# Kernel optimization log

Hardware: AMD Instinct MI355X
Metric: run time of the kernel (lower is better)

The kernel has to match this reference:

```python
import jax, jax.numpy as jnp
import numpy as np

B, T, M, P, Y_DIM = 1024, 128, 256, 256, 1


def setup_inputs() -> dict:
    key = jax.random.key(0)
    ks = jax.random.split(key, 12)
    s = 0.05
    return {
        "Y": jax.random.normal(ks[0], (B, T - 1, Y_DIM), jnp.float32),
        "X_encoded": jax.random.normal(ks[1], (T, B, M), jnp.float32),
        # attention params (torch Linear weight layout: (out, in), no bias)
        "WU_d": jax.random.normal(ks[2], (M, 2 * P + M), jnp.float32) * s,
        "v_d": jax.random.normal(ks[3], (1, M), jnp.float32) * s,
        "Wl": jax.random.normal(ks[4], (1, Y_DIM + M), jnp.float32) * s,
        # LSTM(1, p) params, pytorch gate order i,f,g,o
        "W_ih": jax.random.normal(ks[5], (4 * P, 1), jnp.float32) * s,
        "W_hh": jax.random.normal(ks[6], (4 * P, P), jnp.float32) * s,
        "b_ih": jax.random.normal(ks[7], (4 * P,), jnp.float32) * s,
        "b_hh": jax.random.normal(ks[8], (4 * P,), jnp.float32) * s,
        # output head (with bias)
        "Wb_w": jax.random.normal(ks[9], (P, P + M), jnp.float32) * s,
        "Wb_b": jnp.zeros((P,), jnp.float32),
        "vb_w": jax.random.normal(ks[10], (Y_DIM, P), jnp.float32) * s,
        "vb_b": jnp.zeros((Y_DIM,), jnp.float32),
    }


def _decode(Y, X_encoded, WU_d, v_d, Wl, W_ih, W_hh, b_ih, b_hh, Wb_w, Wb_b, vb_w, vb_b):
    X_bt = jnp.transpose(X_encoded, (1, 0, 2))  # (B, T, m)
    b = Y.shape[0]

    def step(carry, y_t):
        h, c, _ = carry  # h,c: (B, p)
        d = jnp.concatenate([h, c], axis=-1)  # (B, 2p)
        d_rep = jnp.broadcast_to(d[:, None, :], (b, T, 2 * P))
        z = jnp.concatenate([d_rep, X_bt], axis=-1)  # (B, T, 2p+m)
        l = jnp.einsum('btm,om->bto', jnp.tanh(jnp.einsum('btk,mk->btm', z, WU_d)), v_d)[..., 0]  # (B, T)
        beta = jax.nn.softmax(l, axis=1)
        ctx = jnp.einsum('bt,btm->bm', beta, X_bt)  # (B, m)
        y_tilde = jnp.concatenate([y_t, ctx], axis=-1) @ Wl.T  # (B, 1)
        gates = y_tilde @ W_ih.T + h @ W_hh.T + b_ih + b_hh  # (B, 4p)
        i_g, f_g, g_g, o_g = jnp.split(gates, 4, axis=-1)
        c_new = jax.nn.sigmoid(f_g) * c + jax.nn.sigmoid(i_g) * jnp.tanh(g_g)
        h_new = jax.nn.sigmoid(o_g) * jnp.tanh(c_new)
        return (h_new, c_new, ctx), None

    init = (jnp.zeros((b, P), Y.dtype), jnp.zeros((b, P), Y.dtype), jnp.zeros((b, M), Y.dtype))
    (h, c, ctx), _ = jax.lax.scan(step, init, jnp.transpose(Y, (1, 0, 2)))  # scan over T-1 steps
    hc = jnp.concatenate([h, ctx], axis=-1)  # (B, p+m)
    return (hc @ Wb_w.T + Wb_b) @ vb_w.T + vb_b  # (B, y_dim)


def reference(Y, X_encoded, WU_d, v_d, Wl, W_ih, W_hh, b_ih, b_hh, Wb_w, Wb_b, vb_w, vb_b):
    return _decode(Y, X_encoded, WU_d, v_d, Wl, W_ih, W_hh, b_ih, b_hh, Wb_w, Wb_b, vb_w, vb_b)
```

## Files before the change

### kernel.cpp

```cpp
#include <hip/hip_runtime.h>


#define B_SZ 1024
#define T_SZ 128
#define M_SZ 256
#define NSTEP 127

typedef __attribute__((ext_vector_type(8))) short short8;
typedef __attribute__((ext_vector_type(4))) float f32x4;

__device__ __forceinline__ float bf2f_lo(unsigned u) {
  return __builtin_bit_cast(float, u << 16);
}
__device__ __forceinline__ float bf2f_hi(unsigned u) {
  return __builtin_bit_cast(float, u & 0xffff0000u);
}
__device__ __forceinline__ unsigned short f2bf(float f) {
  unsigned u = __builtin_bit_cast(unsigned, f);
  u = (u + 0x7fffu + ((u >> 16) & 1u)) >> 16;
  return (unsigned short)u;
}
__device__ __forceinline__ float fexp2(float x) { return __builtin_amdgcn_exp2f(x); }
__device__ __forceinline__ float frcp(float x) { return __builtin_amdgcn_rcpf(x); }
__device__ __forceinline__ float tanh_f(float x) {
  float t = fexp2(x * 2.8853900817779268f);
  return 1.f - 2.f * frcp(t + 1.f);
}
__device__ __forceinline__ float sigm_f(float x) {
  return frcp(1.f + fexp2(x * -1.4426950408889634f));
}
__device__ __forceinline__ short8 as_s8(uint4 u) { return __builtin_bit_cast(short8, u); }

__global__ void prep_w(const float* __restrict__ WU_d,
                       const float* __restrict__ W_hh,
                       const float* __restrict__ b_ih,
                       const float* __restrict__ b_hh,
                       unsigned short* __restrict__ W1F,
                       unsigned short* __restrict__ W2F,
                       unsigned short* __restrict__ WxF,
                       float* __restrict__ bsum) {
  int i = blockIdx.x * 256 + threadIdx.x;
  if (i < 131072) {
    int j = i & 7, lane = (i >> 3) & 63, ks = (i >> 9) & 15, mt = i >> 13;
    int r = lane & 15, kg = lane >> 4;
    int k = ks * 32 + kg * 8 + j;
    W1F[i] = f2bf(WU_d[(mt * 16 + r) * 768 + k]);
  } else if (i < 131072 + 262144) {
    int i2 = i - 131072;
    int j = i2 & 7, lane = (i2 >> 3) & 63, ks = (i2 >> 9) & 7, jt = i2 >> 12;
    int r = lane & 15, kg = lane >> 4;
    int k = ks * 32 + kg * 8 + j;
    W2F[i2] = f2bf(W_hh[(jt * 16 + r) * 256 + k]);
  } else if (i < 131072 + 262144 + 65536) {
    int i3 = i - (131072 + 262144);
    int j = i3 & 7, lane = (i3 >> 3) & 63, ks = (i3 >> 9) & 7, mt = i3 >> 12;
    int r = lane & 15, kg = lane >> 4;
    int k = 512 + ks * 32 + kg * 8 + j;
    WxF[i3] = f2bf(WU_d[(mt * 16 + r) * 768 + k]);
  } else if (i < 131072 + 262144 + 65536 + 1024) {
    int i4 = i - (131072 + 262144 + 65536);
    bsum[i4] = b_ih[i4] + b_hh[i4];
  }
}

__global__ __launch_bounds__(256, 1) void prep_xw(
    const float* __restrict__ X,
    const unsigned short* __restrict__ WxF,
    const float* __restrict__ Wl,
    unsigned short* __restrict__ XW,
    float* __restrict__ XWl) {
  __shared__ __align__(16) unsigned short XL[128 * 256];
  const int b = blockIdx.x, tid = threadIdx.x;
  for (int i = tid; i < 128 * 256; i += 256) {
    int t = i >> 8, k = i & 255;
    XL[i] = f2bf(X[(size_t)t * 262144 + (size_t)b * 256 + k]);
  }
  __syncthreads();
  const int wave = tid >> 6, lane = tid & 63, r = lane & 15, kg = lane >> 4;
  for (int tt = 0; tt < 8; ++tt) {
    uint4 a[8];
#pragma unroll
    for (int ks = 0; ks < 8; ++ks)
      a[ks] = *(const uint4*)&XL[(tt * 16 + r) * 256 + ks * 32 + kg * 8];
#pragma unroll
    for (int mtl = 0; mtl < 4; ++mtl) {
      const int mt = wave * 4 + mtl;
      f32x4 acc = {0.f, 0.f, 0.f, 0.f};
#pragma unroll
      for (int ks = 0; ks < 8; ++ks) {
        uint4 braw = *(const uint4*)(WxF + ((size_t)(mt * 8 + ks) * 64 + lane) * 8);
        acc = __builtin_amdgcn_mfma_f32_16x16x32_bf16(as_s8(a[ks]), as_s8(braw), acc, 0, 0, 0);
      }
#pragma unroll
      for (int rr = 0; rr < 4; ++rr) {
        int trow = tt * 16 + kg * 4 + rr;
        XW[(size_t)b * 32768 + trow * 256 + mt * 16 + r] = f2bf(acc[rr]);
      }
    }
  }
  float wl4[4];
#pragma unroll
  for (int j = 0; j < 4; ++j) wl4[j] = Wl[1 + lane * 4 + j];
  for (int t = wave * 32; t < wave * 32 + 32; ++t) {
    uint2 q = *(const uint2*)&XL[t * 256 + lane * 4];
    float s = wl4[0] * bf2f_lo(q.x) + wl4[1] * bf2f_hi(q.x) +
              wl4[2] * bf2f_lo(q.y) + wl4[3] * bf2f_hi(q.y);
#pragma unroll
    for (int off = 1; off < 64; off <<= 1) s += __shfl_xor(s, off, 64);
    if (lane == 0) XWl[b * 128 + t] = s;
  }
}

__global__ __launch_bounds__(1024, 4) void scan_k(
    const float* __restrict__ Yg,
    const float* __restrict__ X,
    const unsigned short* __restrict__ XW,
    const float* __restrict__ XWl,
    const unsigned short* __restrict__ W1F,
    const unsigned short* __restrict__ W2F,
    const float* __restrict__ bsum,
    const float* __restrict__ v_d,
    const float* __restrict__ Wl,
    const float* __restrict__ W_ih,
    const float* __restrict__ Wb_w,
    const float* __restrict__ Wb_b,
    const float* __restrict__ vb_w,
    const float* __restrict__ vb_b,
    float* __restrict__ outp) {
  __shared__ __align__(16) unsigned short hcbf[16][520];
  __shared__ __align__(16) float dWL[4][256];
  __shared__ float gL[4][1024];
  __shared__ float lL[4][128];
  __shared__ float betaL[4][128];
  __shared__ float ctxW[4][4][256];
  __shared__ float ctxL[4][256];
  __shared__ float ytL[4];

  const int tid = threadIdx.x;
  const int wave = tid >> 6;
  const int lane = tid & 63;
  const int r = lane & 15;
  const int kg = lane >> 4;
  const int b0 = blockIdx.x * 4;
  const int bb = wave >> 2;
  const int tw = wave & 3;
  const int lp = tid & 255;
  const int lb = tid >> 8;
  const int m8 = (lane & 31) * 8;
  const int th = lane >> 5;

  for (int i = tid; i < 16 * 520; i += 1024) (&hcbf[0][0])[i] = 0;

  float v8[8];
#pragma unroll
  for (int j = 0; j < 8; ++j) v8[j] = v_d[m8 + j];
  float wih4g[4], bs4g[4];
#pragma unroll
  for (int g = 0; g < 4; ++g) { wih4g[g] = W_ih[g * 256 + lp]; bs4g[g] = bsum[g * 256 + lp]; }
  const float wl0 = Wl[0];
  float c_reg = 0.f;

  const unsigned short* XWb = XW + (size_t)(b0 + bb) * (T_SZ * M_SZ);
  const float* Yb = Yg + (size_t)(b0 + wave) * NSTEP;
  const float* XWlb = XWl + (size_t)(b0 + wave) * T_SZ;

  __syncthreads();

  for (int step = 0; step < NSTEP; ++step) {
    {
      const int mt = wave;
      f32x4 acc = {0.f, 0.f, 0.f, 0.f};
      const unsigned short* bp = W1F + ((size_t)(mt * 16) * 64 + lane) * 8;
#pragma unroll
      for (int ks = 0; ks < 16; ++ks) {
        uint4 a = *(const uint4*)&hcbf[r][ks * 32 + kg * 8];
        uint4 braw = *(const uint4*)(bp + (size_t)ks * 512);
        acc = __builtin_amdgcn_mfma_f32_16x16x32_bf16(as_s8(a), as_s8(braw), acc, 0, 0, 0);
      }
      if (kg == 0) {
#pragma unroll
        for (int rr = 0; rr < 4; ++rr) dWL[rr][mt * 16 + r] = acc[rr];
      }
    }
    __syncthreads();

    {
      float dw8[8];
      *(f32x4*)&dw8[0] = *(const f32x4*)&dWL[bb][m8];
      *(f32x4*)&dw8[4] = *(const f32x4*)&dWL[bb][m8 + 4];
      const unsigned short* p = XWb + (tw * 32 + th) * M_SZ + m8;
#pragma unroll 8
      for (int i = 0; i < 16; ++i) {
        uint4 q = *(const uint4*)(p + i * 512);
        float s = v8[0] * tanh_f(dw8[0] + bf2f_lo(q.x)) + v8[1] * tanh_f(dw8[1] + bf2f_hi(q.x)) +
                  v8[2] * tanh_f(dw8[2] + bf2f_lo(q.y)) + v8[3] * tanh_f(dw8[3] + bf2f_hi(q.y)) +
                  v8[4] * tanh_f(dw8[4] + bf2f_lo(q.z)) + v8[5] * tanh_f(dw8[5] + bf2f_hi(q.z)) +
                  v8[6] * tanh_f(dw8[6] + bf2f_lo(q.w)) + v8[7] * tanh_f(dw8[7] + bf2f_hi(q.w));
#pragma unroll
        for (int off = 1; off < 32; off <<= 1) s += __shfl_xor(s, off, 64);
        if ((lane & 31) == 0) lL[bb][tw * 32 + 2 * i + th] = s;
      }
    }
    __syncthreads();

    if (wave < 4) {
      float l0 = lL[wave][lane], l1 = lL[wave][64 + lane];
      float mx = fmaxf(l0, l1);
#pragma unroll
      for (int off = 1; off < 64; off <<= 1) mx = fmaxf(mx, __shfl_xor(mx, off, 64));
      float e0 = fexp2((l0 - mx) * 1.4426950408889634f);
      float e1 = fexp2((l1 - mx) * 1.4426950408889634f);
      float sm = e0 + e1;
      float yt = e0 * XWlb[lane] + e1 * XWlb[64 + lane];
#pragma unroll
      for (int off = 1; off < 64; off <<= 1) {
        sm += __shfl_xor(sm, off, 64);
        yt += __shfl_xor(yt, off, 64);
      }
      float inv = frcp(sm);
      betaL[wave][lane] = e0 * inv;
      betaL[wave][64 + lane] = e1 * inv;
      if (lane == 0) ytL[wave] = yt * inv + wl0 * Yb[step];
    }

    {
#pragma unroll
      for (int jtl = 0; jtl < 4; ++jtl) {
        const int jt = wave * 4 + jtl;
        f32x4 acc = {0.f, 0.f, 0.f, 0.f};
        const unsigned short* bp = W2F + ((size_t)(jt * 8) * 64 + lane) * 8;
#pragma unroll
        for (int ks = 0; ks < 8; ++ks) {
          uint4 a = *(const uint4*)&hcbf[r][ks * 32 + kg * 8];
          uint4 braw = *(const uint4*)(bp + (size_t)ks * 512);
          acc = __builtin_amdgcn_mfma_f32_16x16x32_bf16(as_s8(a), as_s8(braw), acc, 0, 0, 0);
        }
        if (kg == 0) {
#pragma unroll
          for (int rr = 0; rr < 4; ++rr) gL[rr][jt * 16 + r] = acc[rr];
        }
      }
    }
    __syncthreads();

    if (step == NSTEP - 1) {
      const int m4 = lane * 4;
      f32x4 c4 = {0.f, 0.f, 0.f, 0.f};
      for (int t = tw * 32; t < tw * 32 + 32; ++t) {
        float bta = betaL[bb][t];
        f32x4 x4 = *(const f32x4*)&X[(size_t)t * 262144 + (size_t)(b0 + bb) * 256 + m4];
        c4.x += bta * x4.x;
        c4.y += bta * x4.y;
        c4.z += bta * x4.z;
        c4.w += bta * x4.w;
      }
      *(f32x4*)&ctxW[bb][tw][m4] = c4;
    }

    {
      float yt = ytL[lb];
      float ig = gL[lb][lp] + yt * wih4g[0] + bs4g[0];
      float fg = gL[lb][256 + lp] + yt * wih4g[1] + bs4g[1];
      float gg = gL[lb][512 + lp] + yt * wih4g[2] + bs4g[2];
      float og = gL[lb][768 + lp] + yt * wih4g[3] + bs4g[3];
      float cn = sigm_f(fg) * c_reg + sigm_f(ig) * tanh_f(gg);
      float hn = sigm_f(og) * tanh_f(cn);
      c_reg = cn;
      hcbf[lb][lp] = f2bf(hn);
      hcbf[lb][256 + lp] = f2bf(cn);
    }
    __syncthreads();
  }

  ctxL[lb][lp] = ctxW[lb][0][lp] + ctxW[lb][1][lp] + ctxW[lb][2][lp] + ctxW[lb][3][lp];
  __syncthreads();

  if (wave < 4) {
    const int m4 = lane * 4;
    float h0 = 0.f, h1 = 0.f, h2 = 0.f, h3 = 0.f;
    for (int q = 0; q < 512; ++q) {
      float hcq = (q < 256) ? bf2f_lo((unsigned)hcbf[wave][q]) : ctxL[wave][q - 256];
      const float* wb = Wb_w + (size_t)m4 * 512 + q;
      h0 += hcq * wb[0];
      h1 += hcq * wb[512];
      h2 += hcq * wb[1024];
      h3 += hcq * wb[1536];
    }
    float o = (h0 + Wb_b[m4]) * vb_w[m4] + (h1 + Wb_b[m4 + 1]) * vb_w[m4 + 1] +
              (h2 + Wb_b[m4 + 2]) * vb_w[m4 + 2] + (h3 + Wb_b[m4 + 3]) * vb_w[m4 + 3];
#pragma unroll
    for (int off = 1; off < 64; off <<= 1) o += __shfl_xor(o, off, 64);
    if (lane == 0) outp[b0 + wave] = o + vb_b[0];
  }
}

extern "C" void kernel_launch(void* const* d_in, const int* in_sizes, int n_in,
                              void* d_out, int out_size, void* d_ws, size_t ws_size,
                              hipStream_t stream) {
  const float* Y = (const float*)d_in[0];
  const float* X = (const float*)d_in[1];
  const float* WU_d = (const float*)d_in[2];
  const float* v_d = (const float*)d_in[3];
  const float* Wl = (const float*)d_in[4];
  const float* W_ih = (const float*)d_in[5];
  const float* W_hh = (const float*)d_in[6];
  const float* b_ih = (const float*)d_in[7];
  const float* b_hh = (const float*)d_in[8];
  const float* Wb_w = (const float*)d_in[9];
  const float* Wb_b = (const float*)d_in[10];
  const float* vb_w = (const float*)d_in[11];
  const float* vb_b = (const float*)d_in[12];

  char* ws = (char*)d_ws;
  unsigned short* XW = (unsigned short*)(ws + 0);
  float* XWl = (float*)(ws + 67108864);
  unsigned short* W1F = (unsigned short*)(ws + 67633152);
  unsigned short* W2F = (unsigned short*)(ws + 67895296);
  unsigned short* WxF = (unsigned short*)(ws + 68419584);
  float* bsum = (float*)(ws + 68550656);

  prep_w<<<1796, 256, 0, stream>>>(WU_d, W_hh, b_ih, b_hh, W1F, W2F, WxF, bsum);
  prep_xw<<<1024, 256, 0, stream>>>(X, WxF, Wl, XW, XWl);
  scan_k<<<256, 1024, 0, stream>>>(Y, X, XW, XWl, W1F, W2F, bsum, v_d, Wl, W_ih,
                                   Wb_w, Wb_b, vb_w, vb_b, (float*)d_out);
}
```

Measured before the change: 6.008 ms.

## Process two batch rows per block to launch 512 scan blocks

Each 1024-thread scan block now handles 2 batch rows instead of 4, doubling the grid to 512 blocks so all CUs on the device get work. Eight waves now split the 128 time positions per row. Y and XWl per-row values are preloaded into shared memory, and XW and X streaming reads use nontemporal loads. The trade-off is that the per-step MFMA work on W1F/W2F is repeated for fewer rows, so the weight traffic per row roughly doubles and half the MFMA tile rows are wasted.

```diff
diff --git a/kernel.cpp b/kernel.cpp
--- a/kernel.cpp
+++ b/kernel.cpp
@@ -8,6 +8,7 @@
 
 typedef __attribute__((ext_vector_type(8))) short short8;
 typedef __attribute__((ext_vector_type(4))) float f32x4;
+typedef __attribute__((ext_vector_type(4))) unsigned int u32x4;
 
 __device__ __forceinline__ float bf2f_lo(unsigned u) {
   return __builtin_bit_cast(float, u << 16);
@@ -111,7 +112,7 @@
   }
 }
 
-__global__ __launch_bounds__(1024, 4) void scan_k(
+__global__ __launch_bounds__(1024, 8) void scan_k(
     const float* __restrict__ Yg,
     const float* __restrict__ X,
     const unsigned short* __restrict__ XW,
@@ -128,28 +129,38 @@
     const float* __restrict__ vb_b,
     float* __restrict__ outp) {
   __shared__ __align__(16) unsigned short hcbf[16][520];
-  __shared__ __align__(16) float dWL[4][256];
-  __shared__ float gL[4][1024];
-  __shared__ float lL[4][128];
-  __shared__ float betaL[4][128];
-  __shared__ float ctxW[4][4][256];
-  __shared__ float ctxL[4][256];
-  __shared__ float ytL[4];
+  __shared__ __align__(16) float dWL[2][256];
+  __shared__ float gL[2][1024];
+  __shared__ float lL[2][128];
+  __shared__ float betaL[2][128];
+  __shared__ float ctxW[2][8][256];
+  __shared__ float ctxL[2][256];
+  __shared__ float YL[2][128];
+  __shared__ float XWlL[2][128];
+  __shared__ float ytL[2];
 
   const int tid = threadIdx.x;
   const int wave = tid >> 6;
   const int lane = tid & 63;
   const int r = lane & 15;
   const int kg = lane >> 4;
-  const int b0 = blockIdx.x * 4;
-  const int bb = wave >> 2;
-  const int tw = wave & 3;
+  const int b0 = blockIdx.x * 2;
+  const int bb = wave >> 3;
+  const int tw = wave & 7;
   const int lp = tid & 255;
   const int lb = tid >> 8;
   const int m8 = (lane & 31) * 8;
   const int th = lane >> 5;
 
   for (int i = tid; i < 16 * 520; i += 1024) (&hcbf[0][0])[i] = 0;
+  if (tid < 254) {
+    int b2 = tid / 127, st = tid % 127;
+    YL[b2][st] = Yg[(size_t)(b0 + b2) * NSTEP + st];
+  }
+  if (tid >= 512 && tid < 768) {
+    int i2 = tid - 512, b2 = i2 >> 7, t = i2 & 127;
+    XWlL[b2][t] = XWl[(size_t)(b0 + b2) * T_SZ + t];
+  }
 
   float v8[8];
 #pragma unroll
@@ -161,8 +172,6 @@
   float c_reg = 0.f;
 
   const unsigned short* XWb = XW + (size_t)(b0 + bb) * (T_SZ * M_SZ);
-  const float* Yb = Yg + (size_t)(b0 + wave) * NSTEP;
-  const float* XWlb = XWl + (size_t)(b0 + wave) * T_SZ;
 
   __syncthreads();
 
@@ -178,8 +187,8 @@
         acc = __builtin_amdgcn_mfma_f32_16x16x32_bf16(as_s8(a), as_s8(braw), acc, 0, 0, 0);
       }
       if (kg == 0) {
-#pragma unroll
-        for (int rr = 0; rr < 4; ++rr) dWL[rr][mt * 16 + r] = acc[rr];
+        dWL[0][mt * 16 + r] = acc[0];
+        dWL[1][mt * 16 + r] = acc[1];
       }
     }
     __syncthreads();
@@ -188,22 +197,22 @@
       float dw8[8];
       *(f32x4*)&dw8[0] = *(const f32x4*)&dWL[bb][m8];
       *(f32x4*)&dw8[4] = *(const f32x4*)&dWL[bb][m8 + 4];
-      const unsigned short* p = XWb + (tw * 32 + th) * M_SZ + m8;
-#pragma unroll 8
-      for (int i = 0; i < 16; ++i) {
-        uint4 q = *(const uint4*)(p + i * 512);
+      const unsigned short* p = XWb + (tw * 16 + th) * M_SZ + m8;
+#pragma unroll
+      for (int i = 0; i < 8; ++i) {
+        u32x4 q = __builtin_nontemporal_load((const u32x4*)(p + i * 512));
         float s = v8[0] * tanh_f(dw8[0] + bf2f_lo(q.x)) + v8[1] * tanh_f(dw8[1] + bf2f_hi(q.x)) +
                   v8[2] * tanh_f(dw8[2] + bf2f_lo(q.y)) + v8[3] * tanh_f(dw8[3] + bf2f_hi(q.y)) +
                   v8[4] * tanh_f(dw8[4] + bf2f_lo(q.z)) + v8[5] * tanh_f(dw8[5] + bf2f_hi(q.z)) +
                   v8[6] * tanh_f(dw8[6] + bf2f_lo(q.w)) + v8[7] * tanh_f(dw8[7] + bf2f_hi(q.w));
 #pragma unroll
         for (int off = 1; off < 32; off <<= 1) s += __shfl_xor(s, off, 64);
-        if ((lane & 31) == 0) lL[bb][tw * 32 + 2 * i + th] = s;
+        if ((lane & 31) == 0) lL[bb][tw * 16 + 2 * i + th] = s;
       }
     }
     __syncthreads();
 
-    if (wave < 4) {
+    if (wave < 2) {
       float l0 = lL[wave][lane], l1 = lL[wave][64 + lane];
       float mx = fmaxf(l0, l1);
 #pragma unroll
@@ -211,7 +220,7 @@
       float e0 = fexp2((l0 - mx) * 1.4426950408889634f);
       float e1 = fexp2((l1 - mx) * 1.4426950408889634f);
       float sm = e0 + e1;
-      float yt = e0 * XWlb[lane] + e1 * XWlb[64 + lane];
+      float yt = e0 * XWlL[wave][lane] + e1 * XWlL[wave][64 + lane];
 #pragma unroll
       for (int off = 1; off < 64; off <<= 1) {
         sm += __shfl_xor(sm, off, 64);
@@ -220,7 +229,7 @@
       float inv = frcp(sm);
       betaL[wave][lane] = e0 * inv;
       betaL[wave][64 + lane] = e1 * inv;
-      if (lane == 0) ytL[wave] = yt * inv + wl0 * Yb[step];
+      if (lane == 0) ytL[wave] = yt * inv + wl0 * YL[wave][step];
     }
 
     {
@@ -236,8 +245,8 @@
           acc = __builtin_amdgcn_mfma_f32_16x16x32_bf16(as_s8(a), as_s8(braw), acc, 0, 0, 0);
         }
         if (kg == 0) {
-#pragma unroll
-          for (int rr = 0; rr < 4; ++rr) gL[rr][jt * 16 + r] = acc[rr];
+          gL[0][jt * 16 + r] = acc[0];
+          gL[1][jt * 16 + r] = acc[1];
         }
       }
     }
@@ -246,9 +255,10 @@
     if (step == NSTEP - 1) {
       const int m4 = lane * 4;
       f32x4 c4 = {0.f, 0.f, 0.f, 0.f};
-      for (int t = tw * 32; t < tw * 32 + 32; ++t) {
+      for (int t = tw * 16; t < tw * 16 + 16; ++t) {
         float bta = betaL[bb][t];
-        f32x4 x4 = *(const f32x4*)&X[(size_t)t * 262144 + (size_t)(b0 + bb) * 256 + m4];
+        f32x4 x4 = __builtin_nontemporal_load(
+            (const f32x4*)&X[(size_t)t * 262144 + (size_t)(b0 + bb) * 256 + m4]);
         c4.x += bta * x4.x;
         c4.y += bta * x4.y;
         c4.z += bta * x4.z;
@@ -257,7 +267,7 @@
       *(f32x4*)&ctxW[bb][tw][m4] = c4;
     }
 
-    {
+    if (tid < 512) {
       float yt = ytL[lb];
       float ig = gL[lb][lp] + yt * wih4g[0] + bs4g[0];
       float fg = gL[lb][256 + lp] + yt * wih4g[1] + bs4g[1];
@@ -272,10 +282,15 @@
     __syncthreads();
   }
 
-  ctxL[lb][lp] = ctxW[lb][0][lp] + ctxW[lb][1][lp] + ctxW[lb][2][lp] + ctxW[lb][3][lp];
+  if (tid < 512) {
+    float s = 0.f;
+#pragma unroll
+    for (int w = 0; w < 8; ++w) s += ctxW[lb][w][lp];
+    ctxL[lb][lp] = s;
+  }
   __syncthreads();
 
-  if (wave < 4) {
+  if (wave < 2) {
     const int m4 = lane * 4;
     float h0 = 0.f, h1 = 0.f, h2 = 0.f, h3 = 0.f;
     for (int q = 0; q < 512; ++q) {
@@ -321,6 +336,6 @@
 
   prep_w<<<1796, 256, 0, stream>>>(WU_d, W_hh, b_ih, b_hh, W1F, W2F, WxF, bsum);
   prep_xw<<<1024, 256, 0, stream>>>(X, WxF, Wl, XW, XWl);
-  scan_k<<<256, 1024, 0, stream>>>(Y, X, XW, XWl, W1F, W2F, bsum, v_d, Wl, W_ih,
+  scan_k<<<512, 1024, 0, stream>>>(Y, X, XW, XWl, W1F, W2F, bsum, v_d, Wl, W_ih,
                                    Wb_w, Wb_b, vb_w, vb_b, (float*)d_out);
 }
```

New measurement: 14.63 ms. 2.44x slower.
